# Optimization experiments

Measured on AMD Instinct MI355X. Metric: run time of the kernel, lower is better.

Reference implementation:

```python
import jax, jax.numpy as jnp
import numpy as np

N_NODES = 50000
N_EDGES = 800000
D_IN = 128
D_HID = 128
D_OUT = 128


def gcn_conv(x, W, b, src, dst, n_nodes):
    """PyG GCNConv: sym-normalized A+I aggregation, then bias.
    messages flow src -> dst; self-loops handled analytically."""
    h = x @ W  # [N, F_out]
    ones = jnp.ones(src.shape[0], dtype=h.dtype)
    deg = jax.ops.segment_sum(ones, dst, num_segments=n_nodes) + 1.0  # +1 self-loop
    dinv = jax.lax.rsqrt(deg)  # deg^-1/2
    norm = dinv[src] * dinv[dst]  # [E]
    agg = jax.ops.segment_sum(h[src] * norm[:, None], dst, num_segments=n_nodes)
    out = agg + h * (dinv * dinv)[:, None]  # self-loop term: dinv[i]^2 * h[i]
    return out + b


def setup_inputs() -> dict:
    key = jax.random.key(0)
    ks = jax.random.split(key, 12)
    x = jax.random.normal(ks[0], (N_NODES, D_IN), dtype=jnp.float32)
    edge_index = jax.random.randint(ks[1], (2, N_EDGES), 0, N_NODES, dtype=jnp.int64)

    def lin(k, fi, fo):
        s = 1.0 / np.sqrt(fi)
        return jax.random.uniform(k, (fi, fo), jnp.float32, -s, s)

    return {
        "x": x,
        "edge_index": edge_index,
        "W1": lin(ks[2], D_IN, D_HID), "b1": jnp.zeros((D_HID,), jnp.float32),
        "W2": lin(ks[3], D_HID, D_HID), "b2": jnp.zeros((D_HID,), jnp.float32),
        "W3": lin(ks[4], D_HID, D_OUT), "b3": jnp.zeros((D_OUT,), jnp.float32),
        "Wm1": lin(ks[5], 2 * D_HID, D_HID), "bm1": jnp.zeros((D_HID,), jnp.float32),
        "Wm2": lin(ks[6], D_HID, D_HID), "bm2": jnp.zeros((D_HID,), jnp.float32),
    }


def reference(x, edge_index, W1, b1, W2, b2, W3, b3, Wm1, bm1, Wm2, bm2):
    src, dst = edge_index[0], edge_index[1]
    n = x.shape[0]
    h = jax.nn.relu(gcn_conv(x, W1, b1, src, dst, n))
    h = jax.nn.relu(gcn_conv(h, W2, b2, src, dst, n))
    h = gcn_conv(h, W3, b3, src, dst, n)
    # edge head: gather node pairs, concat, 2-layer MLP
    ef = jnp.concatenate([h[src], h[dst]], axis=1)  # [E, 2*hidden]
    es = jax.nn.relu(ef @ Wm1 + bm1) @ Wm2 + bm2  # [E, hidden]
    return jnp.squeeze(es)
```

## Files before the change

### kernel.cpp

```cpp
#include <hip/hip_runtime.h>
#include <stdint.h>

typedef __attribute__((ext_vector_type(8))) short bf16x8;
typedef __attribute__((ext_vector_type(4))) float f32x4;

static __device__ __forceinline__ unsigned short f2b(float f) {
    unsigned int u = __float_as_uint(f);
    unsigned int r = u + 0x7fffu + ((u >> 16) & 1u);
    return (unsigned short)(r >> 16);
}
static __device__ __forceinline__ float b2f(unsigned short u) {
    return __uint_as_float((unsigned int)u << 16);
}
static __device__ __forceinline__ f32x4 b2f4(ushort4 u) {
    f32x4 r;
    r[0] = b2f(u.x); r[1] = b2f(u.y); r[2] = b2f(u.z); r[3] = b2f(u.w);
    return r;
}


__global__ void count_deg(const int* __restrict__ dst, int E, int* __restrict__ counts) {
    int e = blockIdx.x * 256 + threadIdx.x;
    if (e < E) atomicAdd(&counts[dst[e]], 1);
}

__global__ void scan_s1(const int* __restrict__ counts, int N,
                        int* __restrict__ rowstart, float* __restrict__ dinv,
                        int* __restrict__ psum) {
    __shared__ int wsum[16];
    int tid = threadIdx.x, wave = tid >> 6, lane = tid & 63;
    int i = blockIdx.x * 1024 + tid;
    int c = (i < N) ? counts[i] : 0;
    int x = c;
    #pragma unroll
    for (int off = 1; off < 64; off <<= 1) {
        int v = __shfl_up(x, off);
        if (lane >= off) x += v;
    }
    if (lane == 63) wsum[wave] = x;
    __syncthreads();
    int pre = 0, tot = 0;
    #pragma unroll
    for (int w = 0; w < 16; ++w) {
        int s = wsum[w];
        tot += s;
        if (w < wave) pre += s;
    }
    if (i < N) {
        rowstart[i] = pre + x - c;
        dinv[i] = rsqrtf((float)c + 1.0f);
    }
    if (tid == 0) psum[blockIdx.x] = tot;
}

__global__ void scan_s2(int* __restrict__ psum, int nchunk,
                        int* __restrict__ rowstart, int N) {
    __shared__ int wsum[16];
    int tid = threadIdx.x, wave = tid >> 6, lane = tid & 63;
    int v = (tid < nchunk) ? psum[tid] : 0;
    int x = v;
    #pragma unroll
    for (int off = 1; off < 64; off <<= 1) {
        int s = __shfl_up(x, off);
        if (lane >= off) x += s;
    }
    if (lane == 63) wsum[wave] = x;
    __syncthreads();
    int pre = 0, tot = 0;
    #pragma unroll
    for (int w = 0; w < 16; ++w) {
        int s = wsum[w];
        tot += s;
        if (w < wave) pre += s;
    }
    if (tid < nchunk) psum[tid] = pre + x - v;
    if (tid == 0) rowstart[N] = tot;
}

__global__ void scan_s3(int* __restrict__ rowstart, const int* __restrict__ psum,
                        int N, int* __restrict__ cursor) {
    int i = blockIdx.x * 1024 + threadIdx.x;
    if (i < N) {
        int r = rowstart[i] + psum[blockIdx.x];
        rowstart[i] = r;
        cursor[i] = r;
    }
}

__global__ void fill_csr(const int* __restrict__ src, const int* __restrict__ dst, int E,
                         int* __restrict__ cursor, const float* __restrict__ dinv,
                         int2* __restrict__ csr_sn, int* __restrict__ csr_dst,
                         int* __restrict__ csr_eid) {
    int e = blockIdx.x * 256 + threadIdx.x;
    if (e < E) {
        int d = dst[e], s = src[e];
        int p = atomicAdd(&cursor[d], 1);
        float nrm = dinv[s] * dinv[d];
        csr_sn[p] = make_int2(s, __float_as_int(nrm));
        csr_dst[p] = d;
        csr_eid[p] = e;
    }
}


template <int IN_F32>
__global__ __launch_bounds__(256) void node_mfma(const void* __restrict__ inp,
                                                 const float* __restrict__ W,
                                                 unsigned short* __restrict__ outb, int N) {
    __shared__ __align__(16) unsigned short hl[64][136];
    int tid = threadIdx.x;
    int wid = tid >> 6, lane = tid & 63;
    int lg = lane >> 4, l15 = lane & 15;
    int tilebase = blockIdx.x * 64;

    bf16x8 a[2][4];
    #pragma unroll
    for (int mt = 0; mt < 2; ++mt) {
        int col = wid * 32 + mt * 16 + l15;
        #pragma unroll
        for (int kk = 0; kk < 4; ++kk) {
            bf16x8 af;
            #pragma unroll
            for (int ee = 0; ee < 8; ++ee)
                af[ee] = (short)f2b(W[(size_t)(kk * 32 + lg * 8 + ee) * 128 + col]);
            a[mt][kk] = af;
        }
    }

    #pragma unroll
    for (int p = 0; p < 4; ++p) {
        int idx = p * 256 + tid;
        int r = idx >> 4, ci = idx & 15;
        int row = tilebase + r;
        if (row >= N) row = N - 1;
        if (IN_F32) {
            const float* ip = (const float*)inp + (size_t)row * 128 + ci * 8;
            f32x4 x0 = *(const f32x4*)ip;
            f32x4 x1 = *(const f32x4*)(ip + 4);
            uint4 v;
            v.x = (unsigned int)f2b(x0[0]) | ((unsigned int)f2b(x0[1]) << 16);
            v.y = (unsigned int)f2b(x0[2]) | ((unsigned int)f2b(x0[3]) << 16);
            v.z = (unsigned int)f2b(x1[0]) | ((unsigned int)f2b(x1[1]) << 16);
            v.w = (unsigned int)f2b(x1[2]) | ((unsigned int)f2b(x1[3]) << 16);
            *(uint4*)&hl[r][ci * 8] = v;
        } else {
            *(uint4*)&hl[r][ci * 8] =
                *(const uint4*)((const unsigned short*)inp + (size_t)row * 128 + ci * 8);
        }
    }
    __syncthreads();

    f32x4 acc[2][4];
    #pragma unroll
    for (int mt = 0; mt < 2; ++mt)
        #pragma unroll
        for (int nt = 0; nt < 4; ++nt) acc[mt][nt] = (f32x4){0.f, 0.f, 0.f, 0.f};
    #pragma unroll
    for (int kk = 0; kk < 4; ++kk) {
        #pragma unroll
        for (int nt = 0; nt < 4; ++nt) {
            bf16x8 b = *(const bf16x8*)&hl[nt * 16 + l15][kk * 32 + lg * 8];
            acc[0][nt] = __builtin_amdgcn_mfma_f32_16x16x32_bf16(a[0][kk], b, acc[0][nt], 0, 0, 0);
            acc[1][nt] = __builtin_amdgcn_mfma_f32_16x16x32_bf16(a[1][kk], b, acc[1][nt], 0, 0, 0);
        }
    }
    #pragma unroll
    for (int mt = 0; mt < 2; ++mt) {
        int j = wid * 32 + mt * 16 + lg * 4;
        #pragma unroll
        for (int nt = 0; nt < 4; ++nt) {
            int node = tilebase + nt * 16 + l15;
            if (node < N) {
                unsigned int u0 = (unsigned int)f2b(acc[mt][nt][0]) | ((unsigned int)f2b(acc[mt][nt][1]) << 16);
                unsigned int u1 = (unsigned int)f2b(acc[mt][nt][2]) | ((unsigned int)f2b(acc[mt][nt][3]) << 16);
                *(uint2*)(outb + (size_t)node * 128 + j) = make_uint2(u0, u1);
            }
        }
    }
}


template <int RELU>
__global__ __launch_bounds__(256) void aggregate(
        const unsigned short* __restrict__ tb, const int* __restrict__ rowstart,
        const int2* __restrict__ csr_sn, const float* __restrict__ dinv,
        const float* __restrict__ bias, unsigned short* __restrict__ hb, int N) {
    int tid = threadIdx.x;
    int node = blockIdx.x * 8 + (tid >> 5);
    if (node >= N) return;
    int c = (tid & 31) * 4;
    float di = dinv[node];
    f32x4 self = b2f4(*(const ushort4*)(tb + (size_t)node * 128 + c));
    f32x4 acc = *(const f32x4*)(bias + c) + (di * di) * self;
    int e = rowstart[node], re = rowstart[node + 1];
    for (; e + 7 < re; e += 8) {
        int2 p0 = csr_sn[e + 0], p1 = csr_sn[e + 1], p2 = csr_sn[e + 2], p3 = csr_sn[e + 3];
        int2 p4 = csr_sn[e + 4], p5 = csr_sn[e + 5], p6 = csr_sn[e + 6], p7 = csr_sn[e + 7];
        ushort4 r0 = *(const ushort4*)(tb + (size_t)p0.x * 128 + c);
        ushort4 r1 = *(const ushort4*)(tb + (size_t)p1.x * 128 + c);
        ushort4 r2 = *(const ushort4*)(tb + (size_t)p2.x * 128 + c);
        ushort4 r3 = *(const ushort4*)(tb + (size_t)p3.x * 128 + c);
        ushort4 r4 = *(const ushort4*)(tb + (size_t)p4.x * 128 + c);
        ushort4 r5 = *(const ushort4*)(tb + (size_t)p5.x * 128 + c);
        ushort4 r6 = *(const ushort4*)(tb + (size_t)p6.x * 128 + c);
        ushort4 r7 = *(const ushort4*)(tb + (size_t)p7.x * 128 + c);
        acc += __int_as_float(p0.y) * b2f4(r0);
        acc += __int_as_float(p1.y) * b2f4(r1);
        acc += __int_as_float(p2.y) * b2f4(r2);
        acc += __int_as_float(p3.y) * b2f4(r3);
        acc += __int_as_float(p4.y) * b2f4(r4);
        acc += __int_as_float(p5.y) * b2f4(r5);
        acc += __int_as_float(p6.y) * b2f4(r6);
        acc += __int_as_float(p7.y) * b2f4(r7);
    }
    for (; e + 3 < re; e += 4) {
        int2 p0 = csr_sn[e + 0], p1 = csr_sn[e + 1], p2 = csr_sn[e + 2], p3 = csr_sn[e + 3];
        ushort4 r0 = *(const ushort4*)(tb + (size_t)p0.x * 128 + c);
        ushort4 r1 = *(const ushort4*)(tb + (size_t)p1.x * 128 + c);
        ushort4 r2 = *(const ushort4*)(tb + (size_t)p2.x * 128 + c);
        ushort4 r3 = *(const ushort4*)(tb + (size_t)p3.x * 128 + c);
        acc += __int_as_float(p0.y) * b2f4(r0);
        acc += __int_as_float(p1.y) * b2f4(r1);
        acc += __int_as_float(p2.y) * b2f4(r2);
        acc += __int_as_float(p3.y) * b2f4(r3);
    }
    for (; e < re; ++e) {
        int2 p0 = csr_sn[e];
        acc += __int_as_float(p0.y) * b2f4(*(const ushort4*)(tb + (size_t)p0.x * 128 + c));
    }
    if (RELU) {
        #pragma unroll
        for (int j = 0; j < 4; ++j) acc[j] = fmaxf(acc[j], 0.f);
    }
    unsigned int u0 = (unsigned int)f2b(acc[0]) | ((unsigned int)f2b(acc[1]) << 16);
    unsigned int u1 = (unsigned int)f2b(acc[2]) | ((unsigned int)f2b(acc[3]) << 16);
    *(uint2*)(hb + (size_t)node * 128 + c) = make_uint2(u0, u1);
}


__global__ __launch_bounds__(256) void uv_gemm(const unsigned short* __restrict__ h3b,
                                               const float* __restrict__ Wm1,
                                               unsigned short* __restrict__ uvb, int N) {
    __shared__ __align__(16) unsigned short hl[64][136];
    int tid = threadIdx.x;
    int wid = tid >> 6, lane = tid & 63;
    int lg = lane >> 4, l15 = lane & 15;
    int tilebase = blockIdx.x * 64;

    bf16x8 a[4][4];
    #pragma unroll
    for (int mt = 0; mt < 4; ++mt) {
        int jc = wid * 64 + mt * 16 + l15;
        int koff = (jc >> 7) * 128;
        int col = jc & 127;
        #pragma unroll
        for (int kk = 0; kk < 4; ++kk) {
            bf16x8 af;
            #pragma unroll
            for (int ee = 0; ee < 8; ++ee)
                af[ee] = (short)f2b(Wm1[(size_t)(koff + kk * 32 + lg * 8 + ee) * 128 + col]);
            a[mt][kk] = af;
        }
    }

    #pragma unroll
    for (int p = 0; p < 4; ++p) {
        int idx = p * 256 + tid;
        int r = idx >> 4, ci = idx & 15;
        int row = tilebase + r;
        if (row >= N) row = N - 1;
        uint4 v = *(const uint4*)(h3b + (size_t)row * 128 + ci * 8);
        *(uint4*)&hl[r][ci * 8] = v;
    }
    __syncthreads();

    f32x4 acc[4][4];
    #pragma unroll
    for (int mt = 0; mt < 4; ++mt)
        #pragma unroll
        for (int nt = 0; nt < 4; ++nt) acc[mt][nt] = (f32x4){0.f, 0.f, 0.f, 0.f};
    #pragma unroll
    for (int kk = 0; kk < 4; ++kk) {
        #pragma unroll
        for (int nt = 0; nt < 4; ++nt) {
            bf16x8 b = *(const bf16x8*)&hl[nt * 16 + l15][kk * 32 + lg * 8];
            #pragma unroll
            for (int mt = 0; mt < 4; ++mt)
                acc[mt][nt] = __builtin_amdgcn_mfma_f32_16x16x32_bf16(a[mt][kk], b, acc[mt][nt], 0, 0, 0);
        }
    }
    #pragma unroll
    for (int mt = 0; mt < 4; ++mt) {
        int jc = wid * 64 + mt * 16 + lg * 4;
        #pragma unroll
        for (int nt = 0; nt < 4; ++nt) {
            int node = tilebase + nt * 16 + l15;
            if (node < N) {
                unsigned int u0 = (unsigned int)f2b(acc[mt][nt][0]) | ((unsigned int)f2b(acc[mt][nt][1]) << 16);
                unsigned int u1 = (unsigned int)f2b(acc[mt][nt][2]) | ((unsigned int)f2b(acc[mt][nt][3]) << 16);
                *(uint2*)(uvb + (size_t)node * 256 + jc) = make_uint2(u0, u1);
            }
        }
    }
}


__global__ __launch_bounds__(256, 3) void edge_head4(
        const unsigned short* __restrict__ uvb, const int2* __restrict__ csr_sn,
        const int* __restrict__ csr_dst, const int* __restrict__ csr_eid,
        const float* __restrict__ bm1, const float* __restrict__ Wm2,
        const float* __restrict__ bm2, float* __restrict__ out, int E, int ntiles) {
    __shared__ __align__(16) unsigned short zl[64][136];
    __shared__ int eid_l[64];
    int tid = threadIdx.x;
    int wid = tid >> 6, lane = tid & 63;
    int lg = lane >> 4, l15 = lane & 15;
    int es = tid >> 4;
    int ci = tid & 15;
    int c0 = ci * 8;

    bf16x8 a2[2][4];
    float b2v[2][4];
    #pragma unroll
    for (int mt = 0; mt < 2; ++mt) {
        int m = wid * 32 + mt * 16 + l15;
        #pragma unroll
        for (int kk = 0; kk < 4; ++kk) {
            bf16x8 af;
            #pragma unroll
            for (int ee = 0; ee < 8; ++ee)
                af[ee] = (short)f2b(Wm2[(size_t)(kk * 32 + lg * 8 + ee) * 128 + m]);
            a2[mt][kk] = af;
        }
        #pragma unroll
        for (int r = 0; r < 4; ++r)
            b2v[mt][r] = bm2[wid * 32 + mt * 16 + lg * 4 + r];
    }
    float bm1v[8];
    #pragma unroll
    for (int j = 0; j < 8; ++j) bm1v[j] = bm1[c0 + j];

    uint4 uuA[4], uuB[4];
    int dA[4], dB[4], eidA[4], eidB[4];

    auto stage = [&](int tile, uint4 (&uu)[4], int (&dd)[4], int (&ee)[4]) {
        #pragma unroll
        for (int p = 0; p < 4; ++p) {
            int slot = tile * 64 + p * 16 + es;
            int cs = (slot < E) ? slot : (E - 1);
            int s = csr_sn[cs].x;
            dd[p] = csr_dst[cs];
            ee[p] = (slot < E) ? csr_eid[cs] : -1;
            uu[p] = *(const uint4*)(uvb + (size_t)s * 256 + c0);
        }
    };

    int t = blockIdx.x;
    if (t < ntiles) stage(t, uuA, dA, eidA);
    for (; t < ntiles; t += gridDim.x) {
        __syncthreads();
        #pragma unroll
        for (int p = 0; p < 4; ++p) {
            uint4 vv = *(const uint4*)(uvb + (size_t)dA[p] * 256 + 128 + c0);
            uint4 uu = uuA[p];
            float z0 = fmaxf(b2f((unsigned short)(uu.x)) + b2f((unsigned short)(vv.x)) + bm1v[0], 0.f);
            float z1 = fmaxf(b2f((unsigned short)(uu.x >> 16)) + b2f((unsigned short)(vv.x >> 16)) + bm1v[1], 0.f);
            float z2 = fmaxf(b2f((unsigned short)(uu.y)) + b2f((unsigned short)(vv.y)) + bm1v[2], 0.f);
            float z3 = fmaxf(b2f((unsigned short)(uu.y >> 16)) + b2f((unsigned short)(vv.y >> 16)) + bm1v[3], 0.f);
            float z4 = fmaxf(b2f((unsigned short)(uu.z)) + b2f((unsigned short)(vv.z)) + bm1v[4], 0.f);
            float z5 = fmaxf(b2f((unsigned short)(uu.z >> 16)) + b2f((unsigned short)(vv.z >> 16)) + bm1v[5], 0.f);
            float z6 = fmaxf(b2f((unsigned short)(uu.w)) + b2f((unsigned short)(vv.w)) + bm1v[6], 0.f);
            float z7 = fmaxf(b2f((unsigned short)(uu.w >> 16)) + b2f((unsigned short)(vv.w >> 16)) + bm1v[7], 0.f);
            uint4 w;
            w.x = (unsigned int)f2b(z0) | ((unsigned int)f2b(z1) << 16);
            w.y = (unsigned int)f2b(z2) | ((unsigned int)f2b(z3) << 16);
            w.z = (unsigned int)f2b(z4) | ((unsigned int)f2b(z5) << 16);
            w.w = (unsigned int)f2b(z6) | ((unsigned int)f2b(z7) << 16);
            *(uint4*)&zl[p * 16 + es][c0] = w;
            if (ci == 0) eid_l[p * 16 + es] = eidA[p];
        }
        int tn = t + gridDim.x;
        bool more = (tn < ntiles);
        if (more) stage(tn, uuB, dB, eidB);
        __syncthreads();

        f32x4 c2[2][4];
        #pragma unroll
        for (int mt = 0; mt < 2; ++mt)
            #pragma unroll
            for (int nt = 0; nt < 4; ++nt) c2[mt][nt] = (f32x4){0.f, 0.f, 0.f, 0.f};
        #pragma unroll
        for (int kk = 0; kk < 4; ++kk) {
            #pragma unroll
            for (int nt = 0; nt < 4; ++nt) {
                bf16x8 b = *(const bf16x8*)&zl[nt * 16 + l15][kk * 32 + lg * 8];
                c2[0][nt] = __builtin_amdgcn_mfma_f32_16x16x32_bf16(a2[0][kk], b, c2[0][nt], 0, 0, 0);
                c2[1][nt] = __builtin_amdgcn_mfma_f32_16x16x32_bf16(a2[1][kk], b, c2[1][nt], 0, 0, 0);
            }
        }
        #pragma unroll
        for (int mt = 0; mt < 2; ++mt) {
            #pragma unroll
            for (int nt = 0; nt < 4; ++nt) {
                int eg = eid_l[nt * 16 + l15];
                if (eg >= 0) {
                    f32x4 o;
                    #pragma unroll
                    for (int r = 0; r < 4; ++r) o[r] = c2[mt][nt][r] + b2v[mt][r];
                    *(f32x4*)(out + (size_t)eg * 128 + wid * 32 + mt * 16 + lg * 4) = o;
                }
            }
        }
        if (more) {
            #pragma unroll
            for (int p = 0; p < 4; ++p) {
                uuA[p] = uuB[p]; dA[p] = dB[p]; eidA[p] = eidB[p];
            }
        }
    }
}


extern "C" void kernel_launch(void* const* d_in, const int* in_sizes, int n_in,
                              void* d_out, int out_size, void* d_ws, size_t ws_size,
                              hipStream_t stream) {
    const float* x  = (const float*)d_in[0];
    const int*   ei = (const int*)d_in[1];
    const float* W1 = (const float*)d_in[2];
    const float* b1 = (const float*)d_in[3];
    const float* W2 = (const float*)d_in[4];
    const float* b2 = (const float*)d_in[5];
    const float* W3 = (const float*)d_in[6];
    const float* b3 = (const float*)d_in[7];
    const float* Wm1 = (const float*)d_in[8];
    const float* bm1 = (const float*)d_in[9];
    const float* Wm2 = (const float*)d_in[10];
    const float* bm2 = (const float*)d_in[11];
    float* out = (float*)d_out;

    const int N = in_sizes[0] / 128;
    const int E = in_sizes[1] / 2;
    const int* src = ei;
    const int* dstp = ei + E;

    uintptr_t base = (uintptr_t)d_ws;
    auto alloc = [&](size_t bytes) -> void* {
        uintptr_t p = base;
        base += (bytes + 255) & ~(uintptr_t)255;
        return (void*)p;
    };
    int*   counts   = (int*)alloc((size_t)(N + 1) * 4);
    int*   rowstart = (int*)alloc((size_t)(N + 1) * 4);
    int*   cursor   = (int*)alloc((size_t)N * 4);
    float* dinv     = (float*)alloc((size_t)N * 4);
    int*   psum     = (int*)alloc(4096);
    int2*  csr_sn   = (int2*)alloc((size_t)E * 8);
    int*   csr_d    = (int*)alloc((size_t)E * 4);
    int*   csr_e    = (int*)alloc((size_t)E * 4);
    unsigned short* tb  = (unsigned short*)alloc((size_t)N * 128 * 2);
    unsigned short* hb  = (unsigned short*)alloc((size_t)N * 128 * 2);
    unsigned short* uvb = (unsigned short*)alloc((size_t)N * 256 * 2);
    (void)ws_size; (void)n_in; (void)out_size;

    hipMemsetAsync(counts, 0, (size_t)(N + 1) * 4, stream);

    int egrid = (E + 255) / 256;
    int nchunk = (N + 1023) / 1024;
    count_deg<<<egrid, 256, 0, stream>>>(dstp, E, counts);
    scan_s1<<<nchunk, 1024, 0, stream>>>(counts, N, rowstart, dinv, psum);
    scan_s2<<<1, 1024, 0, stream>>>(psum, nchunk, rowstart, N);
    scan_s3<<<nchunk, 1024, 0, stream>>>(rowstart, psum, N, cursor);
    fill_csr<<<egrid, 256, 0, stream>>>(src, dstp, E, cursor, dinv, csr_sn, csr_d, csr_e);

    int ggrid = (N + 63) / 64;
    int agrid = (N + 7) / 8;
    node_mfma<1><<<ggrid, 256, 0, stream>>>(x, W1, tb, N);
    aggregate<1><<<agrid, 256, 0, stream>>>(tb, rowstart, csr_sn, dinv, b1, hb, N);
    node_mfma<0><<<ggrid, 256, 0, stream>>>(hb, W2, tb, N);
    aggregate<1><<<agrid, 256, 0, stream>>>(tb, rowstart, csr_sn, dinv, b2, hb, N);
    node_mfma<0><<<ggrid, 256, 0, stream>>>(hb, W3, tb, N);
    aggregate<0><<<agrid, 256, 0, stream>>>(tb, rowstart, csr_sn, dinv, b3, hb, N);

    uv_gemm<<<ggrid, 256, 0, stream>>>(hb, Wm1, uvb, N);

    int ntiles = (E + 63) / 64;
    int hgrid = ntiles < 768 ? ntiles : 768;
    edge_head4<<<hgrid, 256, 0, stream>>>(uvb, csr_sn, csr_d, csr_e, bm1, Wm2, bm2, out, E, ntiles);
}
```

Measured before the change: 427.4 us.

## Fuse degree count with first GEMM, merge scan stages, split aggregation by column halves

```diff
diff --git a/kernel.cpp b/kernel.cpp
--- a/kernel.cpp
+++ b/kernel.cpp
@@ -19,10 +19,81 @@
 }
 
 
-__global__ void count_deg(const int* __restrict__ dst, int E, int* __restrict__ counts) {
-    int e = blockIdx.x * 256 + threadIdx.x;
-    if (e < E) atomicAdd(&counts[dst[e]], 1);
-}
+__global__ __launch_bounds__(256) void count_and_gemm1(
+        const int* __restrict__ dst, int E, int* __restrict__ counts, int ecnt,
+        const float* __restrict__ x, const float* __restrict__ W1,
+        unsigned short* __restrict__ outb, int N) {
+    __shared__ __align__(16) unsigned short hl[64][136];
+    int tid = threadIdx.x;
+    if ((int)blockIdx.x < ecnt) {
+        int e = blockIdx.x * 256 + tid;
+        if (e < E) atomicAdd(&counts[dst[e]], 1);
+        return;
+    }
+    int tilebase = (blockIdx.x - ecnt) * 64;
+    int wid = tid >> 6, lane = tid & 63;
+    int lg = lane >> 4, l15 = lane & 15;
+
+    bf16x8 a[2][4];
+    #pragma unroll
+    for (int mt = 0; mt < 2; ++mt) {
+        int col = wid * 32 + mt * 16 + l15;
+        #pragma unroll
+        for (int kk = 0; kk < 4; ++kk) {
+            bf16x8 af;
+            #pragma unroll
+            for (int ee = 0; ee < 8; ++ee)
+                af[ee] = (short)f2b(W1[(size_t)(kk * 32 + lg * 8 + ee) * 128 + col]);
+            a[mt][kk] = af;
+        }
+    }
+    #pragma unroll
+    for (int p = 0; p < 4; ++p) {
+        int idx = p * 256 + tid;
+        int r = idx >> 4, ci = idx & 15;
+        int row = tilebase + r;
+        if (row >= N) row = N - 1;
+        const float* ip = x + (size_t)row * 128 + ci * 8;
+        f32x4 x0 = *(const f32x4*)ip;
+        f32x4 x1 = *(const f32x4*)(ip + 4);
+        uint4 v;
+        v.x = (unsigned int)f2b(x0[0]) | ((unsigned int)f2b(x0[1]) << 16);
+        v.y = (unsigned int)f2b(x0[2]) | ((unsigned int)f2b(x0[3]) << 16);
+        v.z = (unsigned int)f2b(x1[0]) | ((unsigned int)f2b(x1[1]) << 16);
+        v.w = (unsigned int)f2b(x1[2]) | ((unsigned int)f2b(x1[3]) << 16);
+        *(uint4*)&hl[r][ci * 8] = v;
+    }
+    __syncthreads();
+
+    f32x4 acc[2][4];
+    #pragma unroll
+    for (int mt = 0; mt < 2; ++mt)
+        #pragma unroll
+        for (int nt = 0; nt < 4; ++nt) acc[mt][nt] = (f32x4){0.f, 0.f, 0.f, 0.f};
+    #pragma unroll
+    for (int kk = 0; kk < 4; ++kk) {
+        #pragma unroll
+        for (int nt = 0; nt < 4; ++nt) {
+            bf16x8 b = *(const bf16x8*)&hl[nt * 16 + l15][kk * 32 + lg * 8];
+            acc[0][nt] = __builtin_amdgcn_mfma_f32_16x16x32_bf16(a[0][kk], b, acc[0][nt], 0, 0, 0);
+            acc[1][nt] = __builtin_amdgcn_mfma_f32_16x16x32_bf16(a[1][kk], b, acc[1][nt], 0, 0, 0);
+        }
+    }
+    #pragma unroll
+    for (int mt = 0; mt < 2; ++mt) {
+        int j = wid * 32 + mt * 16 + lg * 4;
+        #pragma unroll
+        for (int nt = 0; nt < 4; ++nt) {
+            int node = tilebase + nt * 16 + l15;
+            if (node < N) {
+                unsigned int u0 = (unsigned int)f2b(acc[mt][nt][0]) | ((unsigned int)f2b(acc[mt][nt][1]) << 16);
+                unsigned int u1 = (unsigned int)f2b(acc[mt][nt][2]) | ((unsigned int)f2b(acc[mt][nt][3]) << 16);
+                *(uint2*)(outb + (size_t)node * 128 + j) = make_uint2(u0, u1);
+            }
+        }
+    }
+}
+
 
 __global__ void scan_s1(const int* __restrict__ counts, int N,
                         int* __restrict__ rowstart, float* __restrict__ dinv,
@@ -53,38 +124,22 @@
     if (tid == 0) psum[blockIdx.x] = tot;
 }
 
-__global__ void scan_s2(int* __restrict__ psum, int nchunk,
-                        int* __restrict__ rowstart, int N) {
-    __shared__ int wsum[16];
-    int tid = threadIdx.x, wave = tid >> 6, lane = tid & 63;
-    int v = (tid < nchunk) ? psum[tid] : 0;
-    int x = v;
-    #pragma unroll
-    for (int off = 1; off < 64; off <<= 1) {
-        int s = __shfl_up(x, off);
-        if (lane >= off) x += s;
-    }
-    if (lane == 63) wsum[wave] = x;
-    __syncthreads();
+__global__ void scan_s23(const int* __restrict__ psum, int nchunk,
+                         int* __restrict__ rowstart, int N, int* __restrict__ cursor) {
+    int b = blockIdx.x;
     int pre = 0, tot = 0;
-    #pragma unroll
-    for (int w = 0; w < 16; ++w) {
-        int s = wsum[w];
+    for (int w = 0; w < nchunk; ++w) {
+        int s = psum[w];
         tot += s;
-        if (w < wave) pre += s;
-    }
-    if (tid < nchunk) psum[tid] = pre + x - v;
-    if (tid == 0) rowstart[N] = tot;
-}
-
-__global__ void scan_s3(int* __restrict__ rowstart, const int* __restrict__ psum,
-                        int N, int* __restrict__ cursor) {
-    int i = blockIdx.x * 1024 + threadIdx.x;
+        if (w < b) pre += s;
+    }
+    int i = b * 1024 + threadIdx.x;
     if (i < N) {
-        int r = rowstart[i] + psum[blockIdx.x];
+        int r = rowstart[i] + pre;
         rowstart[i] = r;
         cursor[i] = r;
     }
+    if (b == 0 && threadIdx.x == 0) rowstart[N] = tot;
 }
 
 __global__ void fill_csr(const int* __restrict__ src, const int* __restrict__ dst, int E,
@@ -103,8 +158,7 @@
 }
 
 
-template <int IN_F32>
-__global__ __launch_bounds__(256) void node_mfma(const void* __restrict__ inp,
+__global__ __launch_bounds__(256) void node_mfma(const unsigned short* __restrict__ inp,
                                                  const float* __restrict__ W,
                                                  unsigned short* __restrict__ outb, int N) {
     __shared__ __align__(16) unsigned short hl[64][136];
@@ -126,27 +180,13 @@
             a[mt][kk] = af;
         }
     }
-
     #pragma unroll
     for (int p = 0; p < 4; ++p) {
         int idx = p * 256 + tid;
         int r = idx >> 4, ci = idx & 15;
         int row = tilebase + r;
         if (row >= N) row = N - 1;
-        if (IN_F32) {
-            const float* ip = (const float*)inp + (size_t)row * 128 + ci * 8;
-            f32x4 x0 = *(const f32x4*)ip;
-            f32x4 x1 = *(const f32x4*)(ip + 4);
-            uint4 v;
-            v.x = (unsigned int)f2b(x0[0]) | ((unsigned int)f2b(x0[1]) << 16);
-            v.y = (unsigned int)f2b(x0[2]) | ((unsigned int)f2b(x0[3]) << 16);
-            v.z = (unsigned int)f2b(x1[0]) | ((unsigned int)f2b(x1[1]) << 16);
-            v.w = (unsigned int)f2b(x1[2]) | ((unsigned int)f2b(x1[3]) << 16);
-            *(uint4*)&hl[r][ci * 8] = v;
-        } else {
-            *(uint4*)&hl[r][ci * 8] =
-                *(const uint4*)((const unsigned short*)inp + (size_t)row * 128 + ci * 8);
-        }
+        *(uint4*)&hl[r][ci * 8] = *(const uint4*)(inp + (size_t)row * 128 + ci * 8);
     }
     __syncthreads();
 
@@ -181,14 +221,15 @@
 
 
 template <int RELU>
-__global__ __launch_bounds__(256) void aggregate(
+__global__ __launch_bounds__(256) void aggregate_half(
         const unsigned short* __restrict__ tb, const int* __restrict__ rowstart,
         const int2* __restrict__ csr_sn, const float* __restrict__ dinv,
-        const float* __restrict__ bias, unsigned short* __restrict__ hb, int N) {
+        const float* __restrict__ bias, unsigned short* __restrict__ hb,
+        int N, int colbase) {
     int tid = threadIdx.x;
-    int node = blockIdx.x * 8 + (tid >> 5);
+    int node = blockIdx.x * 16 + (tid >> 4);
     if (node >= N) return;
-    int c = (tid & 31) * 4;
+    int c = colbase + (tid & 15) * 4;
     float di = dinv[node];
     f32x4 self = b2f4(*(const ushort4*)(tb + (size_t)node * 128 + c));
     f32x4 acc = *(const f32x4*)(bias + c) + (di * di) * self;
@@ -466,20 +507,22 @@
 
     int egrid = (E + 255) / 256;
     int nchunk = (N + 1023) / 1024;
-    count_deg<<<egrid, 256, 0, stream>>>(dstp, E, counts);
+    int ggrid = (N + 63) / 64;
+    int sgrid = (N + 15) / 16;
+
+    count_and_gemm1<<<egrid + ggrid, 256, 0, stream>>>(dstp, E, counts, egrid, x, W1, tb, N);
     scan_s1<<<nchunk, 1024, 0, stream>>>(counts, N, rowstart, dinv, psum);
-    scan_s2<<<1, 1024, 0, stream>>>(psum, nchunk, rowstart, N);
-    scan_s3<<<nchunk, 1024, 0, stream>>>(rowstart, psum, N, cursor);
+    scan_s23<<<nchunk, 1024, 0, stream>>>(psum, nchunk, rowstart, N, cursor);
     fill_csr<<<egrid, 256, 0, stream>>>(src, dstp, E, cursor, dinv, csr_sn, csr_d, csr_e);
 
-    int ggrid = (N + 63) / 64;
-    int agrid = (N + 7) / 8;
-    node_mfma<1><<<ggrid, 256, 0, stream>>>(x, W1, tb, N);
-    aggregate<1><<<agrid, 256, 0, stream>>>(tb, rowstart, csr_sn, dinv, b1, hb, N);
-    node_mfma<0><<<ggrid, 256, 0, stream>>>(hb, W2, tb, N);
-    aggregate<1><<<agrid, 256, 0, stream>>>(tb, rowstart, csr_sn, dinv, b2, hb, N);
-    node_mfma<0><<<ggrid, 256, 0, stream>>>(hb, W3, tb, N);
-    aggregate<0><<<agrid, 256, 0, stream>>>(tb, rowstart, csr_sn, dinv, b3, hb, N);
+    aggregate_half<1><<<sgrid, 256, 0, stream>>>(tb, rowstart, csr_sn, dinv, b1, hb, N, 0);
+    aggregate_half<1><<<sgrid, 256, 0, stream>>>(tb, rowstart, csr_sn, dinv, b1, hb, N, 64);
+    node_mfma<<<ggrid, 256, 0, stream>>>(hb, W2, tb, N);
+    aggregate_half<1><<<sgrid, 256, 0, stream>>>(tb, rowstart, csr_sn, dinv, b2, hb, N, 0);
+    aggregate_half<1><<<sgrid, 256, 0, stream>>>(tb, rowstart, csr_sn, dinv, b2, hb, N, 64);
+    node_mfma<<<ggrid, 256, 0, stream>>>(hb, W3, tb, N);
+    aggregate_half<0><<<sgrid, 256, 0, stream>>>(tb, rowstart, csr_sn, dinv, b3, hb, N, 0);
+    aggregate_half<0><<<sgrid, 256, 0, stream>>>(tb, rowstart, csr_sn, dinv, b3, hb, N, 64);
 
     uv_gemm<<<ggrid, 256, 0, stream>>>(hb, Wm1, uvb, N);
 
```

After: 443.4 us. 3.7% more time.

## Fuse aggregation with next-layer GEMM and merge setup kernels

Applied to the files above, without the earlier changes.

```diff
diff --git a/kernel.cpp b/kernel.cpp
--- a/kernel.cpp
+++ b/kernel.cpp
@@ -19,10 +19,81 @@
 }
 
 
-__global__ void count_deg(const int* __restrict__ dst, int E, int* __restrict__ counts) {
-    int e = blockIdx.x * 256 + threadIdx.x;
-    if (e < E) atomicAdd(&counts[dst[e]], 1);
-}
+__global__ __launch_bounds__(256) void count_and_gemm1(
+        const int* __restrict__ dst, int E, int* __restrict__ counts, int ecnt,
+        const float* __restrict__ x, const float* __restrict__ W1,
+        unsigned short* __restrict__ outb, int N) {
+    __shared__ __align__(16) unsigned short hl[64][136];
+    int tid = threadIdx.x;
+    if ((int)blockIdx.x < ecnt) {
+        int e = blockIdx.x * 256 + tid;
+        if (e < E) atomicAdd(&counts[dst[e]], 1);
+        return;
+    }
+    int tilebase = (blockIdx.x - ecnt) * 64;
+    int wid = tid >> 6, lane = tid & 63;
+    int lg = lane >> 4, l15 = lane & 15;
+
+    bf16x8 a[2][4];
+    #pragma unroll
+    for (int mt = 0; mt < 2; ++mt) {
+        int col = wid * 32 + mt * 16 + l15;
+        #pragma unroll
+        for (int kk = 0; kk < 4; ++kk) {
+            bf16x8 af;
+            #pragma unroll
+            for (int ee = 0; ee < 8; ++ee)
+                af[ee] = (short)f2b(W1[(size_t)(kk * 32 + lg * 8 + ee) * 128 + col]);
+            a[mt][kk] = af;
+        }
+    }
+    #pragma unroll
+    for (int p = 0; p < 4; ++p) {
+        int idx = p * 256 + tid;
+        int r = idx >> 4, ci = idx & 15;
+        int row = tilebase + r;
+        if (row >= N) row = N - 1;
+        const float* ip = x + (size_t)row * 128 + ci * 8;
+        f32x4 x0 = *(const f32x4*)ip;
+        f32x4 x1 = *(const f32x4*)(ip + 4);
+        uint4 v;
+        v.x = (unsigned int)f2b(x0[0]) | ((unsigned int)f2b(x0[1]) << 16);
+        v.y = (unsigned int)f2b(x0[2]) | ((unsigned int)f2b(x0[3]) << 16);
+        v.z = (unsigned int)f2b(x1[0]) | ((unsigned int)f2b(x1[1]) << 16);
+        v.w = (unsigned int)f2b(x1[2]) | ((unsigned int)f2b(x1[3]) << 16);
+        *(uint4*)&hl[r][ci * 8] = v;
+    }
+    __syncthreads();
+
+    f32x4 acc[2][4];
+    #pragma unroll
+    for (int mt = 0; mt < 2; ++mt)
+        #pragma unroll
+        for (int nt = 0; nt < 4; ++nt) acc[mt][nt] = (f32x4){0.f, 0.f, 0.f, 0.f};
+    #pragma unroll
+    for (int kk = 0; kk < 4; ++kk) {
+        #pragma unroll
+        for (int nt = 0; nt < 4; ++nt) {
+            bf16x8 b = *(const bf16x8*)&hl[nt * 16 + l15][kk * 32 + lg * 8];
+            acc[0][nt] = __builtin_amdgcn_mfma_f32_16x16x32_bf16(a[0][kk], b, acc[0][nt], 0, 0, 0);
+            acc[1][nt] = __builtin_amdgcn_mfma_f32_16x16x32_bf16(a[1][kk], b, acc[1][nt], 0, 0, 0);
+        }
+    }
+    #pragma unroll
+    for (int mt = 0; mt < 2; ++mt) {
+        int j = wid * 32 + mt * 16 + lg * 4;
+        #pragma unroll
+        for (int nt = 0; nt < 4; ++nt) {
+            int node = tilebase + nt * 16 + l15;
+            if (node < N) {
+                unsigned int u0 = (unsigned int)f2b(acc[mt][nt][0]) | ((unsigned int)f2b(acc[mt][nt][1]) << 16);
+                unsigned int u1 = (unsigned int)f2b(acc[mt][nt][2]) | ((unsigned int)f2b(acc[mt][nt][3]) << 16);
+                *(uint2*)(outb + (size_t)node * 128 + j) = make_uint2(u0, u1);
+            }
+        }
+    }
+}
+
 
 __global__ void scan_s1(const int* __restrict__ counts, int N,
                         int* __restrict__ rowstart, float* __restrict__ dinv,
@@ -53,38 +124,22 @@
     if (tid == 0) psum[blockIdx.x] = tot;
 }
 
-__global__ void scan_s2(int* __restrict__ psum, int nchunk,
-                        int* __restrict__ rowstart, int N) {
-    __shared__ int wsum[16];
-    int tid = threadIdx.x, wave = tid >> 6, lane = tid & 63;
-    int v = (tid < nchunk) ? psum[tid] : 0;
-    int x = v;
-    #pragma unroll
-    for (int off = 1; off < 64; off <<= 1) {
-        int s = __shfl_up(x, off);
-        if (lane >= off) x += s;
-    }
-    if (lane == 63) wsum[wave] = x;
-    __syncthreads();
+__global__ void scan_s23(const int* __restrict__ psum, int nchunk,
+                         int* __restrict__ rowstart, int N, int* __restrict__ cursor) {
+    int b = blockIdx.x;
     int pre = 0, tot = 0;
-    #pragma unroll
-    for (int w = 0; w < 16; ++w) {
-        int s = wsum[w];
+    for (int w = 0; w < nchunk; ++w) {
+        int s = psum[w];
         tot += s;
-        if (w < wave) pre += s;
-    }
-    if (tid < nchunk) psum[tid] = pre + x - v;
-    if (tid == 0) rowstart[N] = tot;
-}
-
-__global__ void scan_s3(int* __restrict__ rowstart, const int* __restrict__ psum,
-                        int N, int* __restrict__ cursor) {
-    int i = blockIdx.x * 1024 + threadIdx.x;
+        if (w < b) pre += s;
+    }
+    int i = b * 1024 + threadIdx.x;
     if (i < N) {
-        int r = rowstart[i] + psum[blockIdx.x];
+        int r = rowstart[i] + pre;
         rowstart[i] = r;
         cursor[i] = r;
     }
+    if (b == 0 && threadIdx.x == 0) rowstart[N] = tot;
 }
 
 __global__ void fill_csr(const int* __restrict__ src, const int* __restrict__ dst, int E,
@@ -102,203 +157,131 @@
     }
 }
 
-
-template <int IN_F32>
-__global__ __launch_bounds__(256) void node_mfma(const void* __restrict__ inp,
-                                                 const float* __restrict__ W,
-                                                 unsigned short* __restrict__ outb, int N) {
+__global__ void rank_csr(const int* __restrict__ rowstart, const int* __restrict__ csr_dst,
+                         const int2* __restrict__ csr_sn, const int* __restrict__ csr_eid,
+                         int2* __restrict__ csr_sn2, int* __restrict__ csr_eid2, int E) {
+    int p = blockIdx.x * 256 + threadIdx.x;
+    if (p >= E) return;
+    int d = csr_dst[p];
+    int rs = rowstart[d], re = rowstart[d + 1];
+    int my = csr_eid[p];
+    int rank = 0;
+    for (int q = rs; q < re; ++q) rank += (csr_eid[q] < my);
+    csr_sn2[rs + rank] = csr_sn[p];
+    csr_eid2[rs + rank] = my;
+}
+
+
+template <int RELU, int UV>
+__global__ __launch_bounds__(256) void agg_gemm(
+        const unsigned short* __restrict__ tb, const int* __restrict__ rowstart,
+        const int2* __restrict__ csr_sn, const float* __restrict__ dinv,
+        const float* __restrict__ bias, const float* __restrict__ W,
+        unsigned short* __restrict__ outb, int N) {
     __shared__ __align__(16) unsigned short hl[64][136];
+    constexpr int MT = UV ? 4 : 2;
     int tid = threadIdx.x;
+    int tilebase = blockIdx.x * 64;
+
+    int nloc = tid >> 5;
+    int c = (tid & 31) * 4;
+    #pragma unroll 1
+    for (int p = 0; p < 8; ++p) {
+        int node = tilebase + p * 8 + nloc;
+        if (node >= N) node = N - 1;
+        float di = dinv[node];
+        f32x4 self = b2f4(*(const ushort4*)(tb + (size_t)node * 128 + c));
+        f32x4 acc = *(const f32x4*)(bias + c) + (di * di) * self;
+        int e = rowstart[node], re = rowstart[node + 1];
+        for (; e + 7 < re; e += 8) {
+            int2 p0 = csr_sn[e + 0], p1 = csr_sn[e + 1], p2 = csr_sn[e + 2], p3 = csr_sn[e + 3];
+            int2 p4 = csr_sn[e + 4], p5 = csr_sn[e + 5], p6 = csr_sn[e + 6], p7 = csr_sn[e + 7];
+            ushort4 r0 = *(const ushort4*)(tb + (size_t)p0.x * 128 + c);
+            ushort4 r1 = *(const ushort4*)(tb + (size_t)p1.x * 128 + c);
+            ushort4 r2 = *(const ushort4*)(tb + (size_t)p2.x * 128 + c);
+            ushort4 r3 = *(const ushort4*)(tb + (size_t)p3.x * 128 + c);
+            ushort4 r4 = *(const ushort4*)(tb + (size_t)p4.x * 128 + c);
+            ushort4 r5 = *(const ushort4*)(tb + (size_t)p5.x * 128 + c);
+            ushort4 r6 = *(const ushort4*)(tb + (size_t)p6.x * 128 + c);
+            ushort4 r7 = *(const ushort4*)(tb + (size_t)p7.x * 128 + c);
+            acc += __int_as_float(p0.y) * b2f4(r0);
+            acc += __int_as_float(p1.y) * b2f4(r1);
+            acc += __int_as_float(p2.y) * b2f4(r2);
+            acc += __int_as_float(p3.y) * b2f4(r3);
+            acc += __int_as_float(p4.y) * b2f4(r4);
+            acc += __int_as_float(p5.y) * b2f4(r5);
+            acc += __int_as_float(p6.y) * b2f4(r6);
+            acc += __int_as_float(p7.y) * b2f4(r7);
+        }
+        for (; e + 3 < re; e += 4) {
+            int2 p0 = csr_sn[e + 0], p1 = csr_sn[e + 1], p2 = csr_sn[e + 2], p3 = csr_sn[e + 3];
+            ushort4 r0 = *(const ushort4*)(tb + (size_t)p0.x * 128 + c);
+            ushort4 r1 = *(const ushort4*)(tb + (size_t)p1.x * 128 + c);
+            ushort4 r2 = *(const ushort4*)(tb + (size_t)p2.x * 128 + c);
+            ushort4 r3 = *(const ushort4*)(tb + (size_t)p3.x * 128 + c);
+            acc += __int_as_float(p0.y) * b2f4(r0);
+            acc += __int_as_float(p1.y) * b2f4(r1);
+            acc += __int_as_float(p2.y) * b2f4(r2);
+            acc += __int_as_float(p3.y) * b2f4(r3);
+        }
+        for (; e < re; ++e) {
+            int2 p0 = csr_sn[e];
+            acc += __int_as_float(p0.y) * b2f4(*(const ushort4*)(tb + (size_t)p0.x * 128 + c));
+        }
+        if (RELU) {
+            #pragma unroll
+            for (int j = 0; j < 4; ++j) acc[j] = fmaxf(acc[j], 0.f);
+        }
+        unsigned int u0 = (unsigned int)f2b(acc[0]) | ((unsigned int)f2b(acc[1]) << 16);
+        unsigned int u1 = (unsigned int)f2b(acc[2]) | ((unsigned int)f2b(acc[3]) << 16);
+        *(uint2*)&hl[p * 8 + nloc][c] = make_uint2(u0, u1);
+    }
+
     int wid = tid >> 6, lane = tid & 63;
     int lg = lane >> 4, l15 = lane & 15;
-    int tilebase = blockIdx.x * 64;
-
-    bf16x8 a[2][4];
-    #pragma unroll
-    for (int mt = 0; mt < 2; ++mt) {
-        int col = wid * 32 + mt * 16 + l15;
+    bf16x8 a[MT][4];
+    #pragma unroll
+    for (int mt = 0; mt < MT; ++mt) {
+        int jc = wid * (MT * 16) + mt * 16 + l15;
+        int koff = UV ? (jc >> 7) * 128 : 0;
+        int col = jc & 127;
         #pragma unroll
         for (int kk = 0; kk < 4; ++kk) {
             bf16x8 af;
             #pragma unroll
             for (int ee = 0; ee < 8; ++ee)
-                af[ee] = (short)f2b(W[(size_t)(kk * 32 + lg * 8 + ee) * 128 + col]);
+                af[ee] = (short)f2b(W[(size_t)(koff + kk * 32 + lg * 8 + ee) * 128 + col]);
             a[mt][kk] = af;
         }
     }
-
-    #pragma unroll
-    for (int p = 0; p < 4; ++p) {
-        int idx = p * 256 + tid;
-        int r = idx >> 4, ci = idx & 15;
-        int row = tilebase + r;
-        if (row >= N) row = N - 1;
-        if (IN_F32) {
-            const float* ip = (const float*)inp + (size_t)row * 128 + ci * 8;
-            f32x4 x0 = *(const f32x4*)ip;
-            f32x4 x1 = *(const f32x4*)(ip + 4);
-            uint4 v;
-            v.x = (unsigned int)f2b(x0[0]) | ((unsigned int)f2b(x0[1]) << 16);
-            v.y = (unsigned int)f2b(x0[2]) | ((unsigned int)f2b(x0[3]) << 16);
-            v.z = (unsigned int)f2b(x1[0]) | ((unsigned int)f2b(x1[1]) << 16);
-            v.w = (unsigned int)f2b(x1[2]) | ((unsigned int)f2b(x1[3]) << 16);
-            *(uint4*)&hl[r][ci * 8] = v;
-        } else {
-            *(uint4*)&hl[r][ci * 8] =
-                *(const uint4*)((const unsigned short*)inp + (size_t)row * 128 + ci * 8);
-        }
-    }
     __syncthreads();
 
-    f32x4 acc[2][4];
-    #pragma unroll
-    for (int mt = 0; mt < 2; ++mt)
-        #pragma unroll
-        for (int nt = 0; nt < 4; ++nt) acc[mt][nt] = (f32x4){0.f, 0.f, 0.f, 0.f};
+    f32x4 acc2[MT][4];
+    #pragma unroll
+    for (int mt = 0; mt < MT; ++mt)
+        #pragma unroll
+        for (int nt = 0; nt < 4; ++nt) acc2[mt][nt] = (f32x4){0.f, 0.f, 0.f, 0.f};
     #pragma unroll
     for (int kk = 0; kk < 4; ++kk) {
         #pragma unroll
         for (int nt = 0; nt < 4; ++nt) {
             bf16x8 b = *(const bf16x8*)&hl[nt * 16 + l15][kk * 32 + lg * 8];
-            acc[0][nt] = __builtin_amdgcn_mfma_f32_16x16x32_bf16(a[0][kk], b, acc[0][nt], 0, 0, 0);
-            acc[1][nt] = __builtin_amdgcn_mfma_f32_16x16x32_bf16(a[1][kk], b, acc[1][nt], 0, 0, 0);
-        }
-    }
-    #pragma unroll
-    for (int mt = 0; mt < 2; ++mt) {
-        int j = wid * 32 + mt * 16 + lg * 4;
+            #pragma unroll
+            for (int mt = 0; mt < MT; ++mt)
+                acc2[mt][nt] = __builtin_amdgcn_mfma_f32_16x16x32_bf16(a[mt][kk], b, acc2[mt][nt], 0, 0, 0);
+        }
+    }
+    constexpr int OC = UV ? 256 : 128;
+    #pragma unroll
+    for (int mt = 0; mt < MT; ++mt) {
+        int jc = wid * (MT * 16) + mt * 16 + lg * 4;
         #pragma unroll
         for (int nt = 0; nt < 4; ++nt) {
             int node = tilebase + nt * 16 + l15;
             if (node < N) {
-                unsigned int u0 = (unsigned int)f2b(acc[mt][nt][0]) | ((unsigned int)f2b(acc[mt][nt][1]) << 16);
-                unsigned int u1 = (unsigned int)f2b(acc[mt][nt][2]) | ((unsigned int)f2b(acc[mt][nt][3]) << 16);
-                *(uint2*)(outb + (size_t)node * 128 + j) = make_uint2(u0, u1);
-            }
-        }
-    }
-}
-
-
-template <int RELU>
-__global__ __launch_bounds__(256) void aggregate(
-        const unsigned short* __restrict__ tb, const int* __restrict__ rowstart,
-        const int2* __restrict__ csr_sn, const float* __restrict__ dinv,
-        const float* __restrict__ bias, unsigned short* __restrict__ hb, int N) {
-    int tid = threadIdx.x;
-    int node = blockIdx.x * 8 + (tid >> 5);
-    if (node >= N) return;
-    int c = (tid & 31) * 4;
-    float di = dinv[node];
-    f32x4 self = b2f4(*(const ushort4*)(tb + (size_t)node * 128 + c));
-    f32x4 acc = *(const f32x4*)(bias + c) + (di * di) * self;
-    int e = rowstart[node], re = rowstart[node + 1];
-    for (; e + 7 < re; e += 8) {
-        int2 p0 = csr_sn[e + 0], p1 = csr_sn[e + 1], p2 = csr_sn[e + 2], p3 = csr_sn[e + 3];
-        int2 p4 = csr_sn[e + 4], p5 = csr_sn[e + 5], p6 = csr_sn[e + 6], p7 = csr_sn[e + 7];
-        ushort4 r0 = *(const ushort4*)(tb + (size_t)p0.x * 128 + c);
-        ushort4 r1 = *(const ushort4*)(tb + (size_t)p1.x * 128 + c);
-        ushort4 r2 = *(const ushort4*)(tb + (size_t)p2.x * 128 + c);
-        ushort4 r3 = *(const ushort4*)(tb + (size_t)p3.x * 128 + c);
-        ushort4 r4 = *(const ushort4*)(tb + (size_t)p4.x * 128 + c);
-        ushort4 r5 = *(const ushort4*)(tb + (size_t)p5.x * 128 + c);
-        ushort4 r6 = *(const ushort4*)(tb + (size_t)p6.x * 128 + c);
-        ushort4 r7 = *(const ushort4*)(tb + (size_t)p7.x * 128 + c);
-        acc += __int_as_float(p0.y) * b2f4(r0);
-        acc += __int_as_float(p1.y) * b2f4(r1);
-        acc += __int_as_float(p2.y) * b2f4(r2);
-        acc += __int_as_float(p3.y) * b2f4(r3);
-        acc += __int_as_float(p4.y) * b2f4(r4);
-        acc += __int_as_float(p5.y) * b2f4(r5);
-        acc += __int_as_float(p6.y) * b2f4(r6);
-        acc += __int_as_float(p7.y) * b2f4(r7);
-    }
-    for (; e + 3 < re; e += 4) {
-        int2 p0 = csr_sn[e + 0], p1 = csr_sn[e + 1], p2 = csr_sn[e + 2], p3 = csr_sn[e + 3];
-        ushort4 r0 = *(const ushort4*)(tb + (size_t)p0.x * 128 + c);
-        ushort4 r1 = *(const ushort4*)(tb + (size_t)p1.x * 128 + c);
-        ushort4 r2 = *(const ushort4*)(tb + (size_t)p2.x * 128 + c);
-        ushort4 r3 = *(const ushort4*)(tb + (size_t)p3.x * 128 + c);
-        acc += __int_as_float(p0.y) * b2f4(r0);
-        acc += __int_as_float(p1.y) * b2f4(r1);
-        acc += __int_as_float(p2.y) * b2f4(r2);
-        acc += __int_as_float(p3.y) * b2f4(r3);
-    }
-    for (; e < re; ++e) {
-        int2 p0 = csr_sn[e];
-        acc += __int_as_float(p0.y) * b2f4(*(const ushort4*)(tb + (size_t)p0.x * 128 + c));
-    }
-    if (RELU) {
-        #pragma unroll
-        for (int j = 0; j < 4; ++j) acc[j] = fmaxf(acc[j], 0.f);
-    }
-    unsigned int u0 = (unsigned int)f2b(acc[0]) | ((unsigned int)f2b(acc[1]) << 16);
-    unsigned int u1 = (unsigned int)f2b(acc[2]) | ((unsigned int)f2b(acc[3]) << 16);
-    *(uint2*)(hb + (size_t)node * 128 + c) = make_uint2(u0, u1);
-}
-
-
-__global__ __launch_bounds__(256) void uv_gemm(const unsigned short* __restrict__ h3b,
-                                               const float* __restrict__ Wm1,
-                                               unsigned short* __restrict__ uvb, int N) {
-    __shared__ __align__(16) unsigned short hl[64][136];
-    int tid = threadIdx.x;
-    int wid = tid >> 6, lane = tid & 63;
-    int lg = lane >> 4, l15 = lane & 15;
-    int tilebase = blockIdx.x * 64;
-
-    bf16x8 a[4][4];
-    #pragma unroll
-    for (int mt = 0; mt < 4; ++mt) {
-        int jc = wid * 64 + mt * 16 + l15;
-        int koff = (jc >> 7) * 128;
-        int col = jc & 127;
-        #pragma unroll
-        for (int kk = 0; kk < 4; ++kk) {
-            bf16x8 af;
-            #pragma unroll
-            for (int ee = 0; ee < 8; ++ee)
-                af[ee] = (short)f2b(Wm1[(size_t)(koff + kk * 32 + lg * 8 + ee) * 128 + col]);
-            a[mt][kk] = af;
-        }
-    }
-
-    #pragma unroll
-    for (int p = 0; p < 4; ++p) {
-        int idx = p * 256 + tid;
-        int r = idx >> 4, ci = idx & 15;
-        int row = tilebase + r;
-        if (row >= N) row = N - 1;
-        uint4 v = *(const uint4*)(h3b + (size_t)row * 128 + ci * 8);
-        *(uint4*)&hl[r][ci * 8] = v;
-    }
-    __syncthreads();
-
-    f32x4 acc[4][4];
-    #pragma unroll
-    for (int mt = 0; mt < 4; ++mt)
-        #pragma unroll
-        for (int nt = 0; nt < 4; ++nt) acc[mt][nt] = (f32x4){0.f, 0.f, 0.f, 0.f};
-    #pragma unroll
-    for (int kk = 0; kk < 4; ++kk) {
-        #pragma unroll
-        for (int nt = 0; nt < 4; ++nt) {
-            bf16x8 b = *(const bf16x8*)&hl[nt * 16 + l15][kk * 32 + lg * 8];
-            #pragma unroll
-            for (int mt = 0; mt < 4; ++mt)
-                acc[mt][nt] = __builtin_amdgcn_mfma_f32_16x16x32_bf16(a[mt][kk], b, acc[mt][nt], 0, 0, 0);
-        }
-    }
-    #pragma unroll
-    for (int mt = 0; mt < 4; ++mt) {
-        int jc = wid * 64 + mt * 16 + lg * 4;
-        #pragma unroll
-        for (int nt = 0; nt < 4; ++nt) {
-            int node = tilebase + nt * 16 + l15;
-            if (node < N) {
-                unsigned int u0 = (unsigned int)f2b(acc[mt][nt][0]) | ((unsigned int)f2b(acc[mt][nt][1]) << 16);
-                unsigned int u1 = (unsigned int)f2b(acc[mt][nt][2]) | ((unsigned int)f2b(acc[mt][nt][3]) << 16);
-                *(uint2*)(uvb + (size_t)node * 256 + jc) = make_uint2(u0, u1);
+                unsigned int u0 = (unsigned int)f2b(acc2[mt][nt][0]) | ((unsigned int)f2b(acc2[mt][nt][1]) << 16);
+                unsigned int u1 = (unsigned int)f2b(acc2[mt][nt][2]) | ((unsigned int)f2b(acc2[mt][nt][3]) << 16);
+                *(uint2*)(outb + (size_t)node * OC + jc) = make_uint2(u0, u1);
             }
         }
     }
@@ -457,8 +440,10 @@
     int2*  csr_sn   = (int2*)alloc((size_t)E * 8);
     int*   csr_d    = (int*)alloc((size_t)E * 4);
     int*   csr_e    = (int*)alloc((size_t)E * 4);
-    unsigned short* tb  = (unsigned short*)alloc((size_t)N * 128 * 2);
-    unsigned short* hb  = (unsigned short*)alloc((size_t)N * 128 * 2);
+    int2*  csr_sn2  = (int2*)alloc((size_t)E * 8);
+    int*   csr_e2   = (int*)alloc((size_t)E * 4);
+    unsigned short* tb1 = (unsigned short*)alloc((size_t)N * 128 * 2);
+    unsigned short* tb2 = (unsigned short*)alloc((size_t)N * 128 * 2);
     unsigned short* uvb = (unsigned short*)alloc((size_t)N * 256 * 2);
     (void)ws_size; (void)n_in; (void)out_size;
 
@@ -466,24 +451,19 @@
 
     int egrid = (E + 255) / 256;
     int nchunk = (N + 1023) / 1024;
-    count_deg<<<egrid, 256, 0, stream>>>(dstp, E, counts);
+    int ggrid = (N + 63) / 64;
+
+    count_and_gemm1<<<egrid + ggrid, 256, 0, stream>>>(dstp, E, counts, egrid, x, W1, tb1, N);
     scan_s1<<<nchunk, 1024, 0, stream>>>(counts, N, rowstart, dinv, psum);
-    scan_s2<<<1, 1024, 0, stream>>>(psum, nchunk, rowstart, N);
-    scan_s3<<<nchunk, 1024, 0, stream>>>(rowstart, psum, N, cursor);
+    scan_s23<<<nchunk, 1024, 0, stream>>>(psum, nchunk, rowstart, N, cursor);
     fill_csr<<<egrid, 256, 0, stream>>>(src, dstp, E, cursor, dinv, csr_sn, csr_d, csr_e);
-
-    int ggrid = (N + 63) / 64;
-    int agrid = (N + 7) / 8;
-    node_mfma<1><<<ggrid, 256, 0, stream>>>(x, W1, tb, N);
-    aggregate<1><<<agrid, 256, 0, stream>>>(tb, rowstart, csr_sn, dinv, b1, hb, N);
-    node_mfma<0><<<ggrid, 256, 0, stream>>>(hb, W2, tb, N);
-    aggregate<1><<<agrid, 256, 0, stream>>>(tb, rowstart, csr_sn, dinv, b2, hb, N);
-    node_mfma<0><<<ggrid, 256, 0, stream>>>(hb, W3, tb, N);
-    aggregate<0><<<agrid, 256, 0, stream>>>(tb, rowstart, csr_sn, dinv, b3, hb, N);
-
-    uv_gemm<<<ggrid, 256, 0, stream>>>(hb, Wm1, uvb, N);
+    rank_csr<<<egrid, 256, 0, stream>>>(rowstart, csr_d, csr_sn, csr_e, csr_sn2, csr_e2, E);
+
+    agg_gemm<1, 0><<<ggrid, 256, 0, stream>>>(tb1, rowstart, csr_sn2, dinv, b1, W2, tb2, N);
+    agg_gemm<1, 0><<<ggrid, 256, 0, stream>>>(tb2, rowstart, csr_sn2, dinv, b2, W3, tb1, N);
+    agg_gemm<0, 1><<<ggrid, 256, 0, stream>>>(tb1, rowstart, csr_sn2, dinv, b3, Wm1, uvb, N);
 
     int ntiles = (E + 63) / 64;
     int hgrid = ntiles < 768 ? ntiles : 768;
-    edge_head4<<<hgrid, 256, 0, stream>>>(uvb, csr_sn, csr_d, csr_e, bm1, Wm2, bm2, out, E, ntiles);
-}
+    edge_head4<<<hgrid, 256, 0, stream>>>(uvb, csr_sn2, csr_d, csr_e2, bm1, Wm2, bm2, out, E, ntiles);
+}
```

New measurement: 498.8 us. 16.7% more time.
